# Kernel tuning notes

Measured on AMD Instinct MI355X. Metric: run time of the kernel, lower is better.

## Reference

```python
import jax, jax.numpy as jnp
import numpy as np

N_MEM = 10  # number of memory items (loop range in the original)


def setup_inputs() -> dict:
    key = jax.random.key(0)
    k1, k2, k3, k4, k5, k6 = jax.random.split(key, 6)
    feature1 = jax.random.normal(k1, (8, 64, 64, 64), dtype=jnp.float32)
    feature2 = jax.random.normal(k2, (8, 128, 32, 32), dtype=jnp.float32)
    feature3 = jax.random.normal(k3, (8, 256, 16, 16), dtype=jnp.float32)
    # Memory bank: 10 items, each item has one entry per feature scale,
    # shaped exactly like the corresponding feature (torch.dist requires it).
    M1 = jax.random.normal(k4, (N_MEM, 8, 64, 64, 64), dtype=jnp.float32)
    M2 = jax.random.normal(k5, (N_MEM, 8, 128, 32, 32), dtype=jnp.float32)
    M3 = jax.random.normal(k6, (N_MEM, 8, 256, 16, 16), dtype=jnp.float32)
    return {"feature1": feature1, "feature2": feature2, "feature3": feature3,
            "M1": M1, "M2": M2, "M3": M3}


def _frob_dist(f, M):
    # torch.dist(f, M[i]) = ||f - M[i]||_F ; vectorized over the memory axis.
    d2 = jnp.sum((f[None] - M) ** 2, axis=tuple(range(1, M.ndim)))  # [N_MEM]
    return jnp.sqrt(d2)


def reference(feature1, feature2, feature3, M1, M2, M3):
    total = (_frob_dist(feature1, M1)
             + _frob_dist(feature2, M2)
             + _frob_dist(feature3, M3))          # [N_MEM]
    mi_index = jnp.argmin(total)
    mi1 = M1[mi_index]  # [8,64,64,64]
    mi2 = M2[mi_index]  # [8,128,32,32]
    mi3 = M3[mi_index]  # [8,256,16,16]
    CI1 = jnp.concatenate([feature1, mi1], axis=1)
    CI2 = jnp.concatenate([feature2, mi2], axis=1)
    CI3 = jnp.concatenate([feature3, mi3], axis=1)
    return (CI1, CI2, CI3, mi1, mi2, mi3)
```

## Files before the change

kernel.cpp:

```cpp
#include <hip/hip_runtime.h>

#define BLK 256
#define MAXB 512

__global__ void dist_kernel(const float* __restrict__ f1, const float* __restrict__ M1,
                            const float* __restrict__ f2, const float* __restrict__ M2,
                            const float* __restrict__ f3, const float* __restrict__ M3,
                            float* __restrict__ partials) {
    const int pair  = blockIdx.y;
    const int scale = pair >= 20 ? 2 : (pair >= 10 ? 1 : 0);
    const int item  = pair - scale * 10;
    const float* f; const float* M; int n4;
    if (scale == 0)      { f = f1; M = M1; n4 = 524288; }
    else if (scale == 1) { f = f2; M = M2; n4 = 262144; }
    else                 { f = f3; M = M3; n4 = 131072; }
    const int nblocks = n4 >> 10;
    if ((int)blockIdx.x >= nblocks) return;

    const float4* __restrict__ f4 = (const float4*)f;
    const float4* __restrict__ m4 = (const float4*)M + (size_t)item * n4;
    const int tid = blockIdx.x * BLK + threadIdx.x;
    const int S   = nblocks * BLK;

    float4 a0 = f4[tid];
    float4 b0 = m4[tid];
    float4 a1 = f4[tid + S];
    float4 b1 = m4[tid + S];
    float4 a2 = f4[tid + 2 * S];
    float4 b2 = m4[tid + 2 * S];
    float4 a3 = f4[tid + 3 * S];
    float4 b3 = m4[tid + 3 * S];

    float acc = 0.f;
    {
        float dx, dy, dz, dw;
        dx = a0.x - b0.x; dy = a0.y - b0.y; dz = a0.z - b0.z; dw = a0.w - b0.w;
        acc += dx * dx + dy * dy + dz * dz + dw * dw;
        dx = a1.x - b1.x; dy = a1.y - b1.y; dz = a1.z - b1.z; dw = a1.w - b1.w;
        acc += dx * dx + dy * dy + dz * dz + dw * dw;
        dx = a2.x - b2.x; dy = a2.y - b2.y; dz = a2.z - b2.z; dw = a2.w - b2.w;
        acc += dx * dx + dy * dy + dz * dz + dw * dw;
        dx = a3.x - b3.x; dy = a3.y - b3.y; dz = a3.z - b3.z; dw = a3.w - b3.w;
        acc += dx * dx + dy * dy + dz * dz + dw * dw;
    }

    #pragma unroll
    for (int off = 32; off > 0; off >>= 1) acc += __shfl_down(acc, off);

    __shared__ float s[BLK / 64];
    if ((threadIdx.x & 63) == 0) s[threadIdx.x >> 6] = acc;
    __syncthreads();
    if (threadIdx.x == 0)
        partials[pair * MAXB + blockIdx.x] = s[0] + s[1] + s[2] + s[3];
}

__global__ void reduce_argmin_kernel(const float* __restrict__ partials,
                                     int* __restrict__ idx_out) {
    __shared__ float tot[30];
    const int wv = threadIdx.x >> 6, lane = threadIdx.x & 63;
    for (int p = wv; p < 30; p += 4) {
        const int scale = p >= 20 ? 2 : (p >= 10 ? 1 : 0);
        const int nb = MAXB >> scale;
        float s = 0.f;
        for (int i = lane; i < nb; i += 64) s += partials[p * MAXB + i];
        #pragma unroll
        for (int off = 32; off > 0; off >>= 1) s += __shfl_down(s, off);
        if (lane == 0) tot[p] = s;
    }
    __syncthreads();
    if (threadIdx.x == 0) {
        float best = 3.4e38f; int bi = 0;
        for (int i = 0; i < 10; ++i) {
            float t = sqrtf(tot[i]) + sqrtf(tot[10 + i]) + sqrtf(tot[20 + i]);
            if (t < best) { best = t; bi = i; }
        }
        *idx_out = bi;
    }
}

__global__ void gather_kernel(const float* __restrict__ f1, const float* __restrict__ M1,
                              const float* __restrict__ f2, const float* __restrict__ M2,
                              const float* __restrict__ f3, const float* __restrict__ M3,
                              const int* __restrict__ idx_ptr, float* __restrict__ out) {
    const int s = blockIdx.y;
    const float* f; const float* M; int n4, sh; float* CI; float* mi;
    if (s == 0)      { f = f1; M = M1; n4 = 524288; sh = 16; CI = out;           mi = out + 7340032;  }
    else if (s == 1) { f = f2; M = M2; n4 = 262144; sh = 15; CI = out + 4194304; mi = out + 9437184;  }
    else             { f = f3; M = M3; n4 = 131072; sh = 14; CI = out + 6291456; mi = out + 10485760; }
    const int gid = blockIdx.x * BLK + threadIdx.x;
    if (gid >= n4) return;
    const int idx = *idx_ptr;

    const float4* __restrict__ f4 = (const float4*)f;
    const float4* __restrict__ m4 = (const float4*)M + (size_t)idx * n4;
    float4* __restrict__ ci4 = (float4*)CI;
    float4* __restrict__ mi4 = (float4*)mi;

    const int S4 = 1 << sh, mask = S4 - 1;
    const int b = gid >> sh, r = gid & mask;
    float4 va = f4[gid];
    float4 vb = m4[gid];
    const size_t cbase = ((size_t)b << (sh + 1)) + r;
    ci4[cbase]      = va;
    ci4[cbase + S4] = vb;
    mi4[gid]        = vb;
}

extern "C" void kernel_launch(void* const* d_in, const int* in_sizes, int n_in,
                              void* d_out, int out_size, void* d_ws, size_t ws_size,
                              hipStream_t stream) {
    const float* f1 = (const float*)d_in[0];
    const float* f2 = (const float*)d_in[1];
    const float* f3 = (const float*)d_in[2];
    const float* M1 = (const float*)d_in[3];
    const float* M2 = (const float*)d_in[4];
    const float* M3 = (const float*)d_in[5];
    float* out = (float*)d_out;

    float* partials = out + 10485760;
    int* idxp = (int*)d_ws;

    dist_kernel<<<dim3(MAXB, 30), BLK, 0, stream>>>(f1, M1, f2, M2, f3, M3, partials);
    reduce_argmin_kernel<<<1, BLK, 0, stream>>>(partials, idxp);
    gather_kernel<<<dim3(2048, 3), BLK, 0, stream>>>(f1, M1, f2, M2, f3, M3, idxp, out);
}
```

Baseline: 54.46 us.

## Reuse each feature load across all memory items and fuse the feature copy

The distance kernel now gives each thread one feature float4 and has it load the matching float4 from all 10 memory items. It accumulates 10 partial sums in registers and writes per-block partials for every item. Before, each (scale, item) pair had its own block, so the features were re-read ten times. The first half of each CI output is now written inside the distance kernel, so the gather kernel only copies the selected memory item. The cost is more registers per thread and ten separate wave reductions per block.

Measured after the change: 62.39 us. 14.6% more time.

```diff
diff --git a/kernel.cpp b/kernel.cpp
--- a/kernel.cpp
+++ b/kernel.cpp
@@ -1,109 +1,100 @@
 #include <hip/hip_runtime.h>
 
 #define BLK 256
-#define MAXB 512
+#define NBLOCKS 3584
+
 
 __global__ void dist_kernel(const float* __restrict__ f1, const float* __restrict__ M1,
                             const float* __restrict__ f2, const float* __restrict__ M2,
                             const float* __restrict__ f3, const float* __restrict__ M3,
-                            float* __restrict__ partials) {
-    const int pair  = blockIdx.y;
-    const int scale = pair >= 20 ? 2 : (pair >= 10 ? 1 : 0);
-    const int item  = pair - scale * 10;
-    const float* f; const float* M; int n4;
-    if (scale == 0)      { f = f1; M = M1; n4 = 524288; }
-    else if (scale == 1) { f = f2; M = M2; n4 = 262144; }
-    else                 { f = f3; M = M3; n4 = 131072; }
-    const int nblocks = n4 >> 10;
-    if ((int)blockIdx.x >= nblocks) return;
+                            float* __restrict__ out, float* __restrict__ partials) {
+    const int b = blockIdx.x;
+    const float* f; const float* M; int n4, sh, lb; float* CI;
+    if (b < 2048)      { f = f1; M = M1; n4 = 524288; sh = 16; lb = b;        CI = out;           }
+    else if (b < 3072) { f = f2; M = M2; n4 = 262144; sh = 15; lb = b - 2048; CI = out + 4194304; }
+    else               { f = f3; M = M3; n4 = 131072; sh = 14; lb = b - 3072; CI = out + 6291456; }
+    const int tid = lb * BLK + threadIdx.x;
 
     const float4* __restrict__ f4 = (const float4*)f;
-    const float4* __restrict__ m4 = (const float4*)M + (size_t)item * n4;
-    const int tid = blockIdx.x * BLK + threadIdx.x;
-    const int S   = nblocks * BLK;
+    const float4* __restrict__ m4 = (const float4*)M;
 
-    float4 a0 = f4[tid];
-    float4 b0 = m4[tid];
-    float4 a1 = f4[tid + S];
-    float4 b1 = m4[tid + S];
-    float4 a2 = f4[tid + 2 * S];
-    float4 b2 = m4[tid + 2 * S];
-    float4 a3 = f4[tid + 3 * S];
-    float4 b3 = m4[tid + 3 * S];
+    float4 a = f4[tid];
+    float4 mv[10];
+    #pragma unroll
+    for (int i = 0; i < 10; ++i) mv[i] = m4[(size_t)i * n4 + tid];
 
-    float acc = 0.f;
     {
-        float dx, dy, dz, dw;
-        dx = a0.x - b0.x; dy = a0.y - b0.y; dz = a0.z - b0.z; dw = a0.w - b0.w;
-        acc += dx * dx + dy * dy + dz * dz + dw * dw;
-        dx = a1.x - b1.x; dy = a1.y - b1.y; dz = a1.z - b1.z; dw = a1.w - b1.w;
-        acc += dx * dx + dy * dy + dz * dz + dw * dw;
-        dx = a2.x - b2.x; dy = a2.y - b2.y; dz = a2.z - b2.z; dw = a2.w - b2.w;
-        acc += dx * dx + dy * dy + dz * dz + dw * dw;
-        dx = a3.x - b3.x; dy = a3.y - b3.y; dz = a3.z - b3.z; dw = a3.w - b3.w;
-        acc += dx * dx + dy * dy + dz * dz + dw * dw;
+        const int bi = tid >> sh, r = tid & ((1 << sh) - 1);
+        ((float4*)CI)[((size_t)bi << (sh + 1)) + r] = a;
     }
 
+    float acc[10];
     #pragma unroll
-    for (int off = 32; off > 0; off >>= 1) acc += __shfl_down(acc, off);
+    for (int i = 0; i < 10; ++i) {
+        float dx = a.x - mv[i].x, dy = a.y - mv[i].y;
+        float dz = a.z - mv[i].z, dw = a.w - mv[i].w;
+        acc[i] = dx * dx + dy * dy + dz * dz + dw * dw;
+    }
 
-    __shared__ float s[BLK / 64];
-    if ((threadIdx.x & 63) == 0) s[threadIdx.x >> 6] = acc;
+    __shared__ float s[10][4];
+    #pragma unroll
+    for (int i = 0; i < 10; ++i) {
+        float v = acc[i];
+        #pragma unroll
+        for (int off = 32; off > 0; off >>= 1) v += __shfl_down(v, off);
+        if ((threadIdx.x & 63) == 0) s[i][threadIdx.x >> 6] = v;
+    }
     __syncthreads();
-    if (threadIdx.x == 0)
-        partials[pair * MAXB + blockIdx.x] = s[0] + s[1] + s[2] + s[3];
+    if (threadIdx.x < 10)
+        partials[threadIdx.x * NBLOCKS + b] =
+            s[threadIdx.x][0] + s[threadIdx.x][1] + s[threadIdx.x][2] + s[threadIdx.x][3];
 }
 
 __global__ void reduce_argmin_kernel(const float* __restrict__ partials,
                                      int* __restrict__ idx_out) {
-    __shared__ float tot[30];
+    __shared__ float tot[10];
     const int wv = threadIdx.x >> 6, lane = threadIdx.x & 63;
-    for (int p = wv; p < 30; p += 4) {
-        const int scale = p >= 20 ? 2 : (p >= 10 ? 1 : 0);
-        const int nb = MAXB >> scale;
-        float s = 0.f;
-        for (int i = lane; i < nb; i += 64) s += partials[p * MAXB + i];
+    if (wv < 10) {
+        const float* p = partials + wv * NBLOCKS;
+        float s0 = 0.f, s1 = 0.f, s2 = 0.f;
+        for (int i = lane; i < 2048; i += 64) s0 += p[i];
+        for (int i = 2048 + lane; i < 3072; i += 64) s1 += p[i];
+        for (int i = 3072 + lane; i < 3584; i += 64) s2 += p[i];
         #pragma unroll
-        for (int off = 32; off > 0; off >>= 1) s += __shfl_down(s, off);
-        if (lane == 0) tot[p] = s;
+        for (int off = 32; off > 0; off >>= 1) {
+            s0 += __shfl_down(s0, off);
+            s1 += __shfl_down(s1, off);
+            s2 += __shfl_down(s2, off);
+        }
+        if (lane == 0) tot[wv] = sqrtf(s0) + sqrtf(s1) + sqrtf(s2);
     }
     __syncthreads();
     if (threadIdx.x == 0) {
         float best = 3.4e38f; int bi = 0;
         for (int i = 0; i < 10; ++i) {
-            float t = sqrtf(tot[i]) + sqrtf(tot[10 + i]) + sqrtf(tot[20 + i]);
+            float t = tot[i];
             if (t < best) { best = t; bi = i; }
         }
         *idx_out = bi;
     }
 }
 
-__global__ void gather_kernel(const float* __restrict__ f1, const float* __restrict__ M1,
-                              const float* __restrict__ f2, const float* __restrict__ M2,
-                              const float* __restrict__ f3, const float* __restrict__ M3,
-                              const int* __restrict__ idx_ptr, float* __restrict__ out) {
-    const int s = blockIdx.y;
-    const float* f; const float* M; int n4, sh; float* CI; float* mi;
-    if (s == 0)      { f = f1; M = M1; n4 = 524288; sh = 16; CI = out;           mi = out + 7340032;  }
-    else if (s == 1) { f = f2; M = M2; n4 = 262144; sh = 15; CI = out + 4194304; mi = out + 9437184;  }
-    else             { f = f3; M = M3; n4 = 131072; sh = 14; CI = out + 6291456; mi = out + 10485760; }
-    const int gid = blockIdx.x * BLK + threadIdx.x;
-    if (gid >= n4) return;
+__global__ void gather_kernel(const float* __restrict__ M1, const float* __restrict__ M2,
+                              const float* __restrict__ M3, const int* __restrict__ idx_ptr,
+                              float* __restrict__ out) {
+    const int b = blockIdx.x;
+    const float* M; int n4, sh, lb; float* CI; float* mi;
+    if (b < 2048)      { M = M1; n4 = 524288; sh = 16; lb = b;        CI = out;           mi = out + 7340032;  }
+    else if (b < 3072) { M = M2; n4 = 262144; sh = 15; lb = b - 2048; CI = out + 4194304; mi = out + 9437184;  }
+    else               { M = M3; n4 = 131072; sh = 14; lb = b - 3072; CI = out + 6291456; mi = out + 10485760; }
+    const int tid = lb * BLK + threadIdx.x;
     const int idx = *idx_ptr;
 
-    const float4* __restrict__ f4 = (const float4*)f;
-    const float4* __restrict__ m4 = (const float4*)M + (size_t)idx * n4;
-    float4* __restrict__ ci4 = (float4*)CI;
-    float4* __restrict__ mi4 = (float4*)mi;
-
-    const int S4 = 1 << sh, mask = S4 - 1;
-    const int b = gid >> sh, r = gid & mask;
-    float4 va = f4[gid];
-    float4 vb = m4[gid];
-    const size_t cbase = ((size_t)b << (sh + 1)) + r;
-    ci4[cbase]      = va;
-    ci4[cbase + S4] = vb;
-    mi4[gid]        = vb;
+    float4 v = ((const float4*)M)[(size_t)idx * n4 + tid];
+    const int bi = tid >> sh, r = tid & ((1 << sh) - 1);
+    const int S4 = 1 << sh;
+    ((float4*)CI)[((size_t)bi << (sh + 1)) + S4 + r] = v;
+    ((float4*)mi)[tid] = v;
 }
 
 extern "C" void kernel_launch(void* const* d_in, const int* in_sizes, int n_in,
@@ -120,7 +111,7 @@
     float* partials = out + 10485760;
     int* idxp = (int*)d_ws;
 
-    dist_kernel<<<dim3(MAXB, 30), BLK, 0, stream>>>(f1, M1, f2, M2, f3, M3, partials);
-    reduce_argmin_kernel<<<1, BLK, 0, stream>>>(partials, idxp);
-    gather_kernel<<<dim3(2048, 3), BLK, 0, stream>>>(f1, M1, f2, M2, f3, M3, idxp, out);
+    dist_kernel<<<NBLOCKS, BLK, 0, stream>>>(f1, M1, f2, M2, f3, M3, out, partials);
+    reduce_argmin_kernel<<<1, 1024, 0, stream>>>(partials, idxp);
+    gather_kernel<<<NBLOCKS, BLK, 0, stream>>>(M1, M2, M3, idxp, out);
 }
```
